# Performance work log

Hardware: AMD Instinct MI355X
Metric: run time of the kernel (lower is better)

Reference implementation:

```python
import jax, jax.numpy as jnp
import numpy as np

E = 8       # num experts
T = 1024    # num tokens
H = 1024    # hidden dim
I = 1024    # intermediate dim (per gate/up half)


def setup_inputs() -> dict:
    key = jax.random.key(0)
    k1, k2, k3, k4 = jax.random.split(key, 4)
    return {
        "hidden_states": jax.random.normal(k1, (T, H), jnp.float32),
        "router_logits": jax.random.normal(k2, (T, E), jnp.float32),
        # W13 stored pre-transposed as in the module: [E, H, 2*I]
        "W13": jax.random.normal(k3, (E, H, 2 * I), jnp.float32) * 0.02,
        # W2 stored pre-transposed: [E, I, H]
        "W2": jax.random.normal(k4, (E, I, H), jnp.float32) * 0.02,
        "top_k": 2,
    }


def reference(hidden_states, router_logits, W13, W2, top_k):
    num_experts = router_logits.shape[-1]
    # --- routing: topk_softmax (softmax over all experts, then top-k) ---
    probs = jax.nn.softmax(router_logits, axis=-1)            # [T, E]
    w, idx = jax.lax.top_k(probs, top_k)                      # [T, K]
    # renormalize=True path of moe_gather
    w = w / jnp.sum(w, axis=-1, keepdims=True)
    # combine weights per expert: [T, E]
    combine = jnp.sum(jax.nn.one_hot(idx, num_experts, dtype=w.dtype) * w[..., None], axis=1)
    # --- grouped gate-up GEMM + silu_and_mul ---
    h13 = jnp.einsum('th,ehf->tef', hidden_states, W13)       # [T, E, 2I]
    gate, up = jnp.split(h13, 2, axis=-1)                     # each [T, E, I]
    act = jax.nn.silu(gate) * up                              # silu_and_mul
    # --- grouped down GEMM ---
    down = jnp.einsum('tei,eih->teh', act, W2)                # [T, E, H]
    # --- combine (moe_gather) ---
    return jnp.einsum('te,teh->th', combine, down)            # [T, H]
```

## Files before the change

### kernel.cpp

```cpp
#include <hip/hip_runtime.h>
#include <hip/hip_bf16.h>
#include <stdint.h>

#define NE    8
#define NTOK  1024
#define NH    1024
#define NI    1024
#define NPAIR 2048

typedef __attribute__((ext_vector_type(8))) short short8;
typedef __attribute__((ext_vector_type(4))) float f32x4;
typedef unsigned short u16;
typedef unsigned int   u32;

__device__ __forceinline__ u16 f2bf(float x) {
    union { float f; u32 u; } v; v.f = x;
    return (u16)((v.u + 0x7fffu + ((v.u >> 16) & 1u)) >> 16);
}

__device__ __forceinline__ void async_ld16(u16* lds, const u16* g) {
    __builtin_amdgcn_global_load_lds(
        (const __attribute__((address_space(1))) u32*)g,
        (__attribute__((address_space(3))) u32*)lds, 16, 0, 0);
}

__global__ __launch_bounds__(256) void route_kernel(
    const float* __restrict__ logits,
    int* __restrict__ counts, int* __restrict__ pair_tok,
    int2* __restrict__ t2p, float2* __restrict__ t2w)
{
    __shared__ int s_cnt[NE];
    __shared__ int s_base[NE];
    const int tid = threadIdx.x;
    if (tid < NE) s_cnt[tid] = 0;
    __syncthreads();

    int eA[4][2]; int slotA[4][2]; float wA[4][2];

    #pragma unroll
    for (int i = 0; i < 4; i++) {
        const int t = tid * 4 + i;
        float l[NE];
        #pragma unroll
        for (int e = 0; e < NE; e++) l[e] = logits[t * NE + e];
        int i0 = 0;
        #pragma unroll
        for (int e = 1; e < NE; e++) if (l[e] > l[i0]) i0 = e;
        int i1 = -1;
        #pragma unroll
        for (int e = 0; e < NE; e++) {
            if (e == i0) continue;
            if (i1 < 0 || l[e] > l[i1]) i1 = e;
        }
        const float e10 = __expf(l[i1] - l[i0]);
        const float inv = 1.0f / (1.0f + e10);
        eA[i][0] = i0; eA[i][1] = i1;
        wA[i][0] = inv; wA[i][1] = e10 * inv;
        slotA[i][0] = atomicAdd(&s_cnt[i0], 1);
        slotA[i][1] = atomicAdd(&s_cnt[i1], 1);
    }
    __syncthreads();
    if (tid == 0) {
        int acc = 0;
        #pragma unroll
        for (int e = 0; e < NE; e++) { s_base[e] = acc; acc += s_cnt[e]; }
    }
    __syncthreads();
    if (tid < NE) counts[tid] = s_cnt[tid];
    #pragma unroll
    for (int i = 0; i < 4; i++) {
        const int t = tid * 4 + i;
        const int p0 = s_base[eA[i][0]] + slotA[i][0];
        const int p1 = s_base[eA[i][1]] + slotA[i][1];
        pair_tok[p0] = t;
        pair_tok[p1] = t;
        t2p[t] = make_int2(p0, p1);
        t2w[t] = make_float2(wA[i][0], wA[i][1]);
    }
}

__device__ __forceinline__ bool find_tile(
    const int* __restrict__ counts, int tile, int bm, int ntn,
    int& e_o, int& mt_o, int& nt_o, int& cnt_o, int& base_o)
{
    int base = 0;
    #pragma unroll
    for (int e = 0; e < NE; e++) {
        const int cnt = counts[e];
        const int mtiles = (cnt + bm - 1) / bm;
        const int tiles = mtiles * ntn;
        if (tile < tiles) {
            e_o = e; mt_o = tile / ntn; nt_o = tile - (tile / ntn) * ntn;
            cnt_o = cnt; base_o = base; return true;
        }
        tile -= tiles; base += cnt;
    }
    return false;
}

__global__ __launch_bounds__(256) void cvt_x_kernel(
    const float* __restrict__ src, u16* __restrict__ dst)
{
    const int i = blockIdx.x * 256 + threadIdx.x;
    const float4* s = (const float4*)src;
    const float4 a = s[2 * i], b = s[2 * i + 1];
    uint4 o;
    o.x = f2bf(a.x) | ((u32)f2bf(a.y) << 16);
    o.y = f2bf(a.z) | ((u32)f2bf(a.w) << 16);
    o.z = f2bf(b.x) | ((u32)f2bf(b.y) << 16);
    o.w = f2bf(b.z) | ((u32)f2bf(b.w) << 16);
    *(uint4*)(dst + (size_t)i * 8) = o;
}

__global__ __launch_bounds__(256) void cvt_tr_kernel(
    const float* __restrict__ src, u16* __restrict__ dst, int K, int N)
{
    __shared__ float Ts[64][65];
    const int ktiles = K >> 6, ntiles = N >> 6;
    const int tpe = ktiles * ntiles;
    const int e = blockIdx.x / tpe;
    const int rem = blockIdx.x - e * tpe;
    const int kt = rem / ntiles, nt = rem - (rem / ntiles) * ntiles;
    const float* sb = src + ((size_t)e * K + (size_t)kt * 64) * N + nt * 64;
    const int tid = threadIdx.x;

    #pragma unroll
    for (int i = 0; i < 4; i++) {
        const int idx = tid + i * 256;
        const int r = idx >> 4, c = (idx & 15) << 2;
        const float4 v = *(const float4*)(sb + (size_t)r * N + c);
        Ts[r][c + 0] = v.x; Ts[r][c + 1] = v.y;
        Ts[r][c + 2] = v.z; Ts[r][c + 3] = v.w;
    }
    __syncthreads();
    u16* db = dst + ((size_t)e * N + (size_t)nt * 64) * K + kt * 64;
    #pragma unroll
    for (int i = 0; i < 2; i++) {
        const int u = tid + i * 256;
        const int n = u >> 3, k8 = (u & 7) << 3;
        uint4 o;
        o.x = f2bf(Ts[k8 + 0][n]) | ((u32)f2bf(Ts[k8 + 1][n]) << 16);
        o.y = f2bf(Ts[k8 + 2][n]) | ((u32)f2bf(Ts[k8 + 3][n]) << 16);
        o.z = f2bf(Ts[k8 + 4][n]) | ((u32)f2bf(Ts[k8 + 5][n]) << 16);
        o.w = f2bf(Ts[k8 + 6][n]) | ((u32)f2bf(Ts[k8 + 7][n]) << 16);
        *(uint4*)(db + (size_t)n * K + k8) = o;
    }
}

__global__ __launch_bounds__(256) void gemm1_kernel(
    const u16* __restrict__ Xb, const u16* __restrict__ W13t,
    const int* __restrict__ counts, const int* __restrict__ pair_tok,
    u16* __restrict__ act)
{
    int e, mt, nt, cnt, base;
    if (!find_tile(counts, blockIdx.x, 128, NI / 64, e, mt, nt, cnt, base)) return;

    __shared__ u16 As[128 * 32];
    __shared__ u16 Bs[128 * 32];

    const int tid = threadIdx.x;
    const int ct = nt * 64;

    const int ra = tid >> 2, sa = (tid & 3) << 3;
    const int t0 = pair_tok[base + min(mt * 128 + ra, cnt - 1)];
    const int t1 = pair_tok[base + min(mt * 128 + 64 + ra, cnt - 1)];
    const u16* ga0 = Xb + (size_t)t0 * NH + sa;
    const u16* ga1 = Xb + (size_t)t1 * NH + sa;
    u16* la0 = As + tid * 8;
    u16* la1 = As + (tid + 256) * 8;

    const u16* gb0 = W13t + ((size_t)e * 2048 + ct + ra) * 1024 + sa;
    const u16* gb1 = W13t + ((size_t)e * 2048 + 1024 + ct + ra) * 1024 + sa;
    u16* lb0 = Bs + tid * 8;
    u16* lb1 = Bs + (tid + 256) * 8;

    const int lane = tid & 63, w = tid >> 6;
    const int quad = lane >> 4, lid = lane & 15;
    const int rw = w >> 1, cw = w & 1;

    const short8* afp[4];
    const short8* bgp[2];
    const short8* bup[2];
    #pragma unroll
    for (int mi = 0; mi < 4; mi++)
        afp[mi] = (const short8*)(As + (rw * 64 + mi * 16 + lid) * 32 + quad * 8);
    #pragma unroll
    for (int nj = 0; nj < 2; nj++) {
        bgp[nj] = (const short8*)(Bs + (cw * 32 + nj * 16 + lid) * 32 + quad * 8);
        bup[nj] = (const short8*)(Bs + (64 + cw * 32 + nj * 16 + lid) * 32 + quad * 8);
    }

    f32x4 accg[4][2] = {};
    f32x4 accu[4][2] = {};

    for (int k0 = 0; k0 < NH; k0 += 32) {
        async_ld16(la0, ga0 + k0);
        async_ld16(la1, ga1 + k0);
        async_ld16(lb0, gb0 + k0);
        async_ld16(lb1, gb1 + k0);
        __syncthreads();
        short8 a[4], bg[2], bu[2];
        #pragma unroll
        for (int mi = 0; mi < 4; mi++) a[mi] = *afp[mi];
        #pragma unroll
        for (int nj = 0; nj < 2; nj++) { bg[nj] = *bgp[nj]; bu[nj] = *bup[nj]; }
        #pragma unroll
        for (int mi = 0; mi < 4; mi++) {
            #pragma unroll
            for (int nj = 0; nj < 2; nj++) {
                accg[mi][nj] = __builtin_amdgcn_mfma_f32_16x16x32_bf16(a[mi], bg[nj], accg[mi][nj], 0, 0, 0);
                accu[mi][nj] = __builtin_amdgcn_mfma_f32_16x16x32_bf16(a[mi], bu[nj], accu[mi][nj], 0, 0, 0);
            }
        }
        __syncthreads();
    }

    #pragma unroll
    for (int mi = 0; mi < 4; mi++) {
        #pragma unroll
        for (int nj = 0; nj < 2; nj++) {
            const int col = ct + cw * 32 + nj * 16 + lid;
            #pragma unroll
            for (int r = 0; r < 4; r++) {
                const int row = mt * 128 + rw * 64 + mi * 16 + quad * 4 + r;
                if (row < cnt) {
                    const float g = accg[mi][nj][r], u = accu[mi][nj][r];
                    const float s = g / (1.0f + __expf(-g)) * u;
                    act[(size_t)(base + row) * NI + col] = f2bf(s);
                }
            }
        }
    }
}

__global__ __launch_bounds__(256) void gemm2_kernel(
    const u16* __restrict__ act, const u16* __restrict__ W2t,
    const int* __restrict__ counts, float* __restrict__ down)
{
    int e, mt, nt, cnt, base;
    if (!find_tile(counts, blockIdx.x, 64, NH / 128, e, mt, nt, cnt, base)) return;

    __shared__ u16 As[64 * 32];
    __shared__ u16 Bs[128 * 32];

    const int tid = threadIdx.x;
    const int ct = nt * 128;

    const int ra = tid >> 2, sa = (tid & 3) << 3;
    const int prow = base + min(mt * 64 + ra, cnt - 1);
    const u16* ga = act + (size_t)prow * NI + sa;
    u16* la = As + tid * 8;

    const u16* gb0 = W2t + ((size_t)e * 1024 + ct + ra) * NI + sa;
    const u16* gb1 = W2t + ((size_t)e * 1024 + ct + 64 + ra) * NI + sa;
    u16* lb0 = Bs + tid * 8;
    u16* lb1 = Bs + (tid + 256) * 8;

    const int lane = tid & 63, w = tid >> 6;
    const int quad = lane >> 4, lid = lane & 15;

    const short8* afp[4];
    const short8* bfp[2];
    #pragma unroll
    for (int mi = 0; mi < 4; mi++)
        afp[mi] = (const short8*)(As + (mi * 16 + lid) * 32 + quad * 8);
    #pragma unroll
    for (int nj = 0; nj < 2; nj++)
        bfp[nj] = (const short8*)(Bs + (w * 32 + nj * 16 + lid) * 32 + quad * 8);

    f32x4 acc[4][2] = {};

    for (int k0 = 0; k0 < NI; k0 += 32) {
        async_ld16(la, ga + k0);
        async_ld16(lb0, gb0 + k0);
        async_ld16(lb1, gb1 + k0);
        __syncthreads();
        short8 a[4], b[2];
        #pragma unroll
        for (int mi = 0; mi < 4; mi++) a[mi] = *afp[mi];
        #pragma unroll
        for (int nj = 0; nj < 2; nj++) b[nj] = *bfp[nj];
        #pragma unroll
        for (int mi = 0; mi < 4; mi++) {
            #pragma unroll
            for (int nj = 0; nj < 2; nj++)
                acc[mi][nj] = __builtin_amdgcn_mfma_f32_16x16x32_bf16(a[mi], b[nj], acc[mi][nj], 0, 0, 0);
        }
        __syncthreads();
    }

    #pragma unroll
    for (int mi = 0; mi < 4; mi++) {
        #pragma unroll
        for (int nj = 0; nj < 2; nj++) {
            const int col = ct + w * 32 + nj * 16 + lid;
            #pragma unroll
            for (int r = 0; r < 4; r++) {
                const int row = mt * 64 + mi * 16 + quad * 4 + r;
                if (row < cnt)
                    down[(size_t)(base + row) * NH + col] = acc[mi][nj][r];
            }
        }
    }
}

__global__ __launch_bounds__(256) void combine_kernel(
    const float* __restrict__ down, const int2* __restrict__ t2p,
    const float2* __restrict__ t2w, float* __restrict__ out)
{
    const int i = blockIdx.x * 256 + threadIdx.x;
    const int t = i >> 8;
    const int c = (i & 255) << 2;
    const int2 p = t2p[t];
    const float2 wv = t2w[t];
    const float4 d0 = *(const float4*)(down + (size_t)p.x * NH + c);
    const float4 d1 = *(const float4*)(down + (size_t)p.y * NH + c);
    float4 o;
    o.x = wv.x * d0.x + wv.y * d1.x;
    o.y = wv.x * d0.y + wv.y * d1.y;
    o.z = wv.x * d0.z + wv.y * d1.z;
    o.w = wv.x * d0.w + wv.y * d1.w;
    *(float4*)(out + (size_t)t * NH + c) = o;
}

extern "C" void kernel_launch(void* const* d_in, const int* in_sizes, int n_in,
                              void* d_out, int out_size, void* d_ws, size_t ws_size,
                              hipStream_t stream)
{
    const float* X      = (const float*)d_in[0];
    const float* logits = (const float*)d_in[1];
    const float* W13    = (const float*)d_in[2];
    const float* W2     = (const float*)d_in[3];
    float* out = (float*)d_out;

    char* ws = (char*)d_ws;
    int*    counts   = (int*)(ws + 0);
    int*    pair_tok = (int*)(ws + 256);
    int2*   t2p      = (int2*)(ws + 256 + 8192);
    float2* t2w      = (float2*)(ws + 256 + 16384);
    u16*    Xb       = (u16*)(ws + 65536);
    u16*    W13t     = (u16*)(ws + 4194304);
    u16*    W2t      = (u16*)(ws + 4194304 + 33554432);
    u16*    act      = (u16*)(ws + 54525952);
    float*  down     = (float*)(ws + 58720256);

    route_kernel<<<1, 256, 0, stream>>>(logits, counts, pair_tok, t2p, t2w);
    cvt_x_kernel<<<512, 256, 0, stream>>>(X, Xb);
    cvt_tr_kernel<<<NE * 16 * 32, 256, 0, stream>>>(W13, W13t, NH, 2 * NI);
    cvt_tr_kernel<<<NE * 16 * 16, 256, 0, stream>>>(W2, W2t, NI, NH);

    const int grid1 = (NPAIR / 128 + NE - 1) * (NI / 64);
    const int grid2 = (NPAIR / 64 + NE - 1) * (NH / 128);
    gemm1_kernel<<<grid1, 256, 0, stream>>>(Xb, W13t, counts, pair_tok, act);
    gemm2_kernel<<<grid2, 256, 0, stream>>>(act, W2t, counts, down);
    combine_kernel<<<NTOK * NH / 1024, 256, 0, stream>>>(down, t2p, t2w, out);
}
```

Baseline: 196.0 us.

## Double-buffer GEMM LDS loads, swizzle LDS, fuse combine into down GEMM via atomics

Both grouped GEMMs now double-buffer their LDS tiles. The next K-slice's async global-to-LDS loads are issued before computing the current slice, using vmcnt waits and raw barriers. An XOR swizzle on the K-chunk offsets reduces LDS bank conflicts on the fragment reads. The down GEMM is retiled to 128x64 and scatters weighted results straight into the zeroed output with atomicAdd, which removes the fp32 down buffer and the separate combine kernel. The cost is a memset, atomic contention, and summation order that is no longer deterministic.

```diff
diff --git a/kernel.cpp b/kernel.cpp
--- a/kernel.cpp
+++ b/kernel.cpp
@@ -6,6 +6,7 @@
 #define NTOK  1024
 #define NH    1024
 #define NI    1024
+#define N13   2048
 #define NPAIR 2048
 
 typedef __attribute__((ext_vector_type(8))) short short8;
@@ -13,6 +14,10 @@
 typedef unsigned short u16;
 typedef unsigned int   u32;
 
+#define WAIT_VM4 0x0F74
+#define WAIT_VM3 0x0F73
+#define WAIT_VM0 0x0F70
+
 __device__ __forceinline__ u16 f2bf(float x) {
     union { float f; u32 u; } v; v.f = x;
     return (u16)((v.u + 0x7fffu + ((v.u >> 16) & 1u)) >> 16);
@@ -27,7 +32,7 @@
 __global__ __launch_bounds__(256) void route_kernel(
     const float* __restrict__ logits,
     int* __restrict__ counts, int* __restrict__ pair_tok,
-    int2* __restrict__ t2p, float2* __restrict__ t2w)
+    float* __restrict__ pair_w)
 {
     __shared__ int s_cnt[NE];
     __shared__ int s_base[NE];
@@ -70,12 +75,12 @@
     #pragma unroll
     for (int i = 0; i < 4; i++) {
         const int t = tid * 4 + i;
-        const int p0 = s_base[eA[i][0]] + slotA[i][0];
-        const int p1 = s_base[eA[i][1]] + slotA[i][1];
-        pair_tok[p0] = t;
-        pair_tok[p1] = t;
-        t2p[t] = make_int2(p0, p1);
-        t2w[t] = make_float2(wA[i][0], wA[i][1]);
+        #pragma unroll
+        for (int k = 0; k < 2; k++) {
+            const int p = s_base[eA[i][k]] + slotA[i][k];
+            pair_tok[p] = t;
+            pair_w[p]   = wA[i][k];
+        }
     }
 }
 
@@ -155,65 +160,76 @@
     int e, mt, nt, cnt, base;
     if (!find_tile(counts, blockIdx.x, 128, NI / 64, e, mt, nt, cnt, base)) return;
 
-    __shared__ u16 As[128 * 32];
-    __shared__ u16 Bs[128 * 32];
+    __shared__ u16 As[2][128 * 32];
+    __shared__ u16 Bs[2][128 * 32];
 
     const int tid = threadIdx.x;
-    const int ct = nt * 64;
-
-    const int ra = tid >> 2, sa = (tid & 3) << 3;
-    const int t0 = pair_tok[base + min(mt * 128 + ra, cnt - 1)];
-    const int t1 = pair_tok[base + min(mt * 128 + 64 + ra, cnt - 1)];
-    const u16* ga0 = Xb + (size_t)t0 * NH + sa;
-    const u16* ga1 = Xb + (size_t)t1 * NH + sa;
-    u16* la0 = As + tid * 8;
-    u16* la1 = As + (tid + 256) * 8;
-
-    const u16* gb0 = W13t + ((size_t)e * 2048 + ct + ra) * 1024 + sa;
-    const u16* gb1 = W13t + ((size_t)e * 2048 + 1024 + ct + ra) * 1024 + sa;
-    u16* lb0 = Bs + tid * 8;
-    u16* lb1 = Bs + (tid + 256) * 8;
+    const int ct  = nt * 64;
+
+    const int m0 = tid >> 2;
+    const int sw16 = (((tid & 3) ^ (m0 & 3)) << 3);
+    const int t0 = pair_tok[base + min(mt * 128 + m0, cnt - 1)];
+    const int t1 = pair_tok[base + min(mt * 128 + 64 + m0, cnt - 1)];
+    const u16* ga0 = Xb + (size_t)t0 * NH + sw16;
+    const u16* ga1 = Xb + (size_t)t1 * NH + sw16;
+    const u16* gb0 = W13t + ((size_t)e * N13 + ct + m0) * 1024 + sw16;
+    const u16* gb1 = W13t + ((size_t)e * N13 + NI + ct + m0) * 1024 + sw16;
 
     const int lane = tid & 63, w = tid >> 6;
     const int quad = lane >> 4, lid = lane & 15;
     const int rw = w >> 1, cw = w & 1;
-
-    const short8* afp[4];
-    const short8* bgp[2];
-    const short8* bup[2];
+    const int fsw = (quad ^ (lid & 3)) << 3;
+    int aoff[4], bgoff[2], buoff[2];
     #pragma unroll
     for (int mi = 0; mi < 4; mi++)
-        afp[mi] = (const short8*)(As + (rw * 64 + mi * 16 + lid) * 32 + quad * 8);
+        aoff[mi] = (rw * 64 + mi * 16 + lid) * 32 + fsw;
     #pragma unroll
     for (int nj = 0; nj < 2; nj++) {
-        bgp[nj] = (const short8*)(Bs + (cw * 32 + nj * 16 + lid) * 32 + quad * 8);
-        bup[nj] = (const short8*)(Bs + (64 + cw * 32 + nj * 16 + lid) * 32 + quad * 8);
+        bgoff[nj] = (cw * 32 + nj * 16 + lid) * 32 + fsw;
+        buoff[nj] = (64 + cw * 32 + nj * 16 + lid) * 32 + fsw;
     }
 
     f32x4 accg[4][2] = {};
     f32x4 accu[4][2] = {};
 
-    for (int k0 = 0; k0 < NH; k0 += 32) {
-        async_ld16(la0, ga0 + k0);
-        async_ld16(la1, ga1 + k0);
-        async_ld16(lb0, gb0 + k0);
-        async_ld16(lb1, gb1 + k0);
-        __syncthreads();
-        short8 a[4], bg[2], bu[2];
-        #pragma unroll
-        for (int mi = 0; mi < 4; mi++) a[mi] = *afp[mi];
-        #pragma unroll
-        for (int nj = 0; nj < 2; nj++) { bg[nj] = *bgp[nj]; bu[nj] = *bup[nj]; }
-        #pragma unroll
-        for (int mi = 0; mi < 4; mi++) {
-            #pragma unroll
-            for (int nj = 0; nj < 2; nj++) {
-                accg[mi][nj] = __builtin_amdgcn_mfma_f32_16x16x32_bf16(a[mi], bg[nj], accg[mi][nj], 0, 0, 0);
-                accu[mi][nj] = __builtin_amdgcn_mfma_f32_16x16x32_bf16(a[mi], bu[nj], accu[mi][nj], 0, 0, 0);
-            }
-        }
-        __syncthreads();
-    }
+#define ISSUE1(b, k0)                                        \
+    {                                                        \
+        async_ld16(&As[b][tid * 8],         ga0 + (k0));     \
+        async_ld16(&As[b][(tid + 256) * 8], ga1 + (k0));     \
+        async_ld16(&Bs[b][tid * 8],         gb0 + (k0));     \
+        async_ld16(&Bs[b][(tid + 256) * 8], gb1 + (k0));     \
+    }
+#define COMP1(b)                                                               \
+    {                                                                          \
+        short8 av[4], gv[2], uv[2];                                            \
+        _Pragma("unroll") for (int mi = 0; mi < 4; mi++)                       \
+            av[mi] = *(const short8*)&As[b][aoff[mi]];                         \
+        _Pragma("unroll") for (int nj = 0; nj < 2; nj++) {                     \
+            gv[nj] = *(const short8*)&Bs[b][bgoff[nj]];                        \
+            uv[nj] = *(const short8*)&Bs[b][buoff[nj]];                        \
+        }                                                                      \
+        _Pragma("unroll") for (int mi = 0; mi < 4; mi++)                       \
+            _Pragma("unroll") for (int nj = 0; nj < 2; nj++) {                 \
+                accg[mi][nj] = __builtin_amdgcn_mfma_f32_16x16x32_bf16(        \
+                    av[mi], gv[nj], accg[mi][nj], 0, 0, 0);                    \
+                accu[mi][nj] = __builtin_amdgcn_mfma_f32_16x16x32_bf16(        \
+                    av[mi], uv[nj], accu[mi][nj], 0, 0, 0);                    \
+            }                                                                  \
+    }
+
+    ISSUE1(0, 0);
+    int buf = 0;
+    for (int k0 = 32; k0 < NH; k0 += 32) {
+        ISSUE1(buf ^ 1, k0);
+        __builtin_amdgcn_s_waitcnt(WAIT_VM4);
+        __builtin_amdgcn_s_barrier();
+        COMP1(buf);
+        __builtin_amdgcn_s_barrier();
+        buf ^= 1;
+    }
+    __builtin_amdgcn_s_waitcnt(WAIT_VM0);
+    __builtin_amdgcn_s_barrier();
+    COMP1(buf);
 
     #pragma unroll
     for (int mi = 0; mi < 4; mi++) {
@@ -231,96 +247,98 @@
             }
         }
     }
+#undef ISSUE1
+#undef COMP1
 }
 
 __global__ __launch_bounds__(256) void gemm2_kernel(
     const u16* __restrict__ act, const u16* __restrict__ W2t,
-    const int* __restrict__ counts, float* __restrict__ down)
+    const int* __restrict__ counts, const int* __restrict__ pair_tok,
+    const float* __restrict__ pair_w, float* __restrict__ out)
 {
     int e, mt, nt, cnt, base;
-    if (!find_tile(counts, blockIdx.x, 64, NH / 128, e, mt, nt, cnt, base)) return;
-
-    __shared__ u16 As[64 * 32];
-    __shared__ u16 Bs[128 * 32];
+    if (!find_tile(counts, blockIdx.x, 128, NH / 64, e, mt, nt, cnt, base)) return;
+
+    __shared__ u16 As[2][128 * 32];
+    __shared__ u16 Bs[2][64 * 32];
 
     const int tid = threadIdx.x;
-    const int ct = nt * 128;
-
-    const int ra = tid >> 2, sa = (tid & 3) << 3;
-    const int prow = base + min(mt * 64 + ra, cnt - 1);
-    const u16* ga = act + (size_t)prow * NI + sa;
-    u16* la = As + tid * 8;
-
-    const u16* gb0 = W2t + ((size_t)e * 1024 + ct + ra) * NI + sa;
-    const u16* gb1 = W2t + ((size_t)e * 1024 + ct + 64 + ra) * NI + sa;
-    u16* lb0 = Bs + tid * 8;
-    u16* lb1 = Bs + (tid + 256) * 8;
+    const int ct  = nt * 64;
+
+    const int m0 = tid >> 2;
+    const int sw16 = (((tid & 3) ^ (m0 & 3)) << 3);
+    const int p0 = base + min(mt * 128 + m0, cnt - 1);
+    const int p1 = base + min(mt * 128 + 64 + m0, cnt - 1);
+    const u16* ga0 = act + (size_t)p0 * NI + sw16;
+    const u16* ga1 = act + (size_t)p1 * NI + sw16;
+    const u16* gb0 = W2t + ((size_t)e * 1024 + ct + m0) * 1024 + sw16;
 
     const int lane = tid & 63, w = tid >> 6;
     const int quad = lane >> 4, lid = lane & 15;
-
-    const short8* afp[4];
-    const short8* bfp[2];
+    const int rw = w >> 1, cw = w & 1;
+    const int fsw = (quad ^ (lid & 3)) << 3;
+    int aoff[4], boff[2];
     #pragma unroll
     for (int mi = 0; mi < 4; mi++)
-        afp[mi] = (const short8*)(As + (mi * 16 + lid) * 32 + quad * 8);
+        aoff[mi] = (rw * 64 + mi * 16 + lid) * 32 + fsw;
     #pragma unroll
     for (int nj = 0; nj < 2; nj++)
-        bfp[nj] = (const short8*)(Bs + (w * 32 + nj * 16 + lid) * 32 + quad * 8);
+        boff[nj] = (cw * 32 + nj * 16 + lid) * 32 + fsw;
 
     f32x4 acc[4][2] = {};
 
-    for (int k0 = 0; k0 < NI; k0 += 32) {
-        async_ld16(la, ga + k0);
-        async_ld16(lb0, gb0 + k0);
-        async_ld16(lb1, gb1 + k0);
-        __syncthreads();
-        short8 a[4], b[2];
-        #pragma unroll
-        for (int mi = 0; mi < 4; mi++) a[mi] = *afp[mi];
-        #pragma unroll
-        for (int nj = 0; nj < 2; nj++) b[nj] = *bfp[nj];
-        #pragma unroll
-        for (int mi = 0; mi < 4; mi++) {
-            #pragma unroll
-            for (int nj = 0; nj < 2; nj++)
-                acc[mi][nj] = __builtin_amdgcn_mfma_f32_16x16x32_bf16(a[mi], b[nj], acc[mi][nj], 0, 0, 0);
-        }
-        __syncthreads();
-    }
+#define ISSUE2(b, k0)                                        \
+    {                                                        \
+        async_ld16(&As[b][tid * 8],         ga0 + (k0));     \
+        async_ld16(&As[b][(tid + 256) * 8], ga1 + (k0));     \
+        async_ld16(&Bs[b][tid * 8],         gb0 + (k0));     \
+    }
+#define COMP2(b)                                                               \
+    {                                                                          \
+        short8 av[4], bv[2];                                                   \
+        _Pragma("unroll") for (int mi = 0; mi < 4; mi++)                       \
+            av[mi] = *(const short8*)&As[b][aoff[mi]];                         \
+        _Pragma("unroll") for (int nj = 0; nj < 2; nj++)                       \
+            bv[nj] = *(const short8*)&Bs[b][boff[nj]];                         \
+        _Pragma("unroll") for (int mi = 0; mi < 4; mi++)                       \
+            _Pragma("unroll") for (int nj = 0; nj < 2; nj++)                   \
+                acc[mi][nj] = __builtin_amdgcn_mfma_f32_16x16x32_bf16(         \
+                    av[mi], bv[nj], acc[mi][nj], 0, 0, 0);                     \
+    }
+
+    ISSUE2(0, 0);
+    int buf = 0;
+    for (int k0 = 32; k0 < NI; k0 += 32) {
+        ISSUE2(buf ^ 1, k0);
+        __builtin_amdgcn_s_waitcnt(WAIT_VM3);
+        __builtin_amdgcn_s_barrier();
+        COMP2(buf);
+        __builtin_amdgcn_s_barrier();
+        buf ^= 1;
+    }
+    __builtin_amdgcn_s_waitcnt(WAIT_VM0);
+    __builtin_amdgcn_s_barrier();
+    COMP2(buf);
 
     #pragma unroll
     for (int mi = 0; mi < 4; mi++) {
         #pragma unroll
-        for (int nj = 0; nj < 2; nj++) {
-            const int col = ct + w * 32 + nj * 16 + lid;
-            #pragma unroll
-            for (int r = 0; r < 4; r++) {
-                const int row = mt * 64 + mi * 16 + quad * 4 + r;
-                if (row < cnt)
-                    down[(size_t)(base + row) * NH + col] = acc[mi][nj][r];
+        for (int r = 0; r < 4; r++) {
+            const int row = mt * 128 + rw * 64 + mi * 16 + quad * 4 + r;
+            if (row < cnt) {
+                const int p = base + row;
+                const int t = pair_tok[p];
+                const float wgt = pair_w[p];
+                #pragma unroll
+                for (int nj = 0; nj < 2; nj++) {
+                    const int col = ct + cw * 32 + nj * 16 + lid;
+                    atomicAdd(out + (size_t)t * NH + col, wgt * acc[mi][nj][r]);
+                }
             }
         }
     }
-}
-
-__global__ __launch_bounds__(256) void combine_kernel(
-    const float* __restrict__ down, const int2* __restrict__ t2p,
-    const float2* __restrict__ t2w, float* __restrict__ out)
-{
-    const int i = blockIdx.x * 256 + threadIdx.x;
-    const int t = i >> 8;
-    const int c = (i & 255) << 2;
-    const int2 p = t2p[t];
-    const float2 wv = t2w[t];
-    const float4 d0 = *(const float4*)(down + (size_t)p.x * NH + c);
-    const float4 d1 = *(const float4*)(down + (size_t)p.y * NH + c);
-    float4 o;
-    o.x = wv.x * d0.x + wv.y * d1.x;
-    o.y = wv.x * d0.y + wv.y * d1.y;
-    o.z = wv.x * d0.z + wv.y * d1.z;
-    o.w = wv.x * d0.w + wv.y * d1.w;
-    *(float4*)(out + (size_t)t * NH + c) = o;
+#undef ISSUE2
+#undef COMP2
 }
 
 extern "C" void kernel_launch(void* const* d_in, const int* in_sizes, int n_in,
@@ -334,24 +352,22 @@
     float* out = (float*)d_out;
 
     char* ws = (char*)d_ws;
-    int*    counts   = (int*)(ws + 0);
-    int*    pair_tok = (int*)(ws + 256);
-    int2*   t2p      = (int2*)(ws + 256 + 8192);
-    float2* t2w      = (float2*)(ws + 256 + 16384);
-    u16*    Xb       = (u16*)(ws + 65536);
-    u16*    W13t     = (u16*)(ws + 4194304);
-    u16*    W2t      = (u16*)(ws + 4194304 + 33554432);
-    u16*    act      = (u16*)(ws + 54525952);
-    float*  down     = (float*)(ws + 58720256);
-
-    route_kernel<<<1, 256, 0, stream>>>(logits, counts, pair_tok, t2p, t2w);
+    int*   counts   = (int*)(ws + 0);
+    int*   pair_tok = (int*)(ws + 256);
+    float* pair_w   = (float*)(ws + 256 + 8192);
+    u16*   Xb       = (u16*)(ws + 65536);
+    u16*   W13t     = (u16*)(ws + 4194304);
+    u16*   W2t      = (u16*)(ws + 4194304 + 33554432);
+    u16*   act      = (u16*)(ws + 54525952);
+
+    hipMemsetAsync(d_out, 0, (size_t)NTOK * NH * sizeof(float), stream);
+    route_kernel<<<1, 256, 0, stream>>>(logits, counts, pair_tok, pair_w);
     cvt_x_kernel<<<512, 256, 0, stream>>>(X, Xb);
-    cvt_tr_kernel<<<NE * 16 * 32, 256, 0, stream>>>(W13, W13t, NH, 2 * NI);
+    cvt_tr_kernel<<<NE * 16 * 32, 256, 0, stream>>>(W13, W13t, NH, N13);
     cvt_tr_kernel<<<NE * 16 * 16, 256, 0, stream>>>(W2, W2t, NI, NH);
 
     const int grid1 = (NPAIR / 128 + NE - 1) * (NI / 64);
-    const int grid2 = (NPAIR / 64 + NE - 1) * (NH / 128);
+    const int grid2 = (NPAIR / 128 + NE - 1) * (NH / 64);
     gemm1_kernel<<<grid1, 256, 0, stream>>>(Xb, W13t, counts, pair_tok, act);
-    gemm2_kernel<<<grid2, 256, 0, stream>>>(act, W2t, counts, down);
-    combine_kernel<<<NTOK * NH / 1024, 256, 0, stream>>>(down, t2p, t2w, out);
-}
+    gemm2_kernel<<<grid2, 256, 0, stream>>>(act, W2t, counts, pair_tok, pair_w, out);
+}
```

After: 200.2 us. +2.2%, slower.
